# Performance work log

Measured on AMD Instinct MI355X. Metric: run time of the kernel, lower is better.

The kernel has to match this reference:

```python
import jax, jax.numpy as jnp
import numpy as np

EPS = 1e-5
NUM_HEADS = 8
MASK_FILL = -50000.0


def set_norm(X, fmask):
    # Masked "set" layer-norm: mean/var over ALL valid (row, feature) entries
    # of each set jointly. fmask: [B, S, 1] float (1 = valid row).
    D = X.shape[-1]
    cnt = fmask.sum(axis=(1, 2), keepdims=True) * D
    mean = (X * fmask).sum(axis=(1, 2), keepdims=True) / cnt
    var = (((X - mean) ** 2) * fmask).sum(axis=(1, 2), keepdims=True) / cnt
    return (X - mean) / jnp.sqrt(var + EPS) * fmask


def setup_inputs() -> dict:
    key = jax.random.key(0)
    ks = jax.random.split(key, 9)
    B, S, D = 8, 1024, 512
    Q = jax.random.normal(ks[0], (B, S, D), dtype=jnp.float32)
    Q = Q.at[:, 3 * S // 4:, :].set(0.0)
    scale = 0.02
    params = {
        'Wq': jax.random.normal(ks[1], (D, D), jnp.float32) * scale,
        'bq': jnp.zeros((D,), jnp.float32),
        'Wk': jax.random.normal(ks[2], (D, D), jnp.float32) * scale,
        'bk': jnp.zeros((D,), jnp.float32),
        'Wv': jax.random.normal(ks[3], (D, D), jnp.float32) * scale,
        'bv': jnp.zeros((D,), jnp.float32),
        'Wo': jax.random.normal(ks[4], (D, D), jnp.float32) * scale,
        'bo': jnp.zeros((D,), jnp.float32),
    }
    return {'Q': Q, **params}


def reference(Q, Wq, bq, Wk, bk, Wv, bv, Wo, bo):
    B, S, D = Q.shape
    H = NUM_HEADS
    hd = D // H

    # row mask: row is valid if any feature is nonzero
    row_valid = jnp.any(Q != 0, axis=-1, keepdims=True)      # [B, S, 1] bool
    fmask = row_valid.astype(Q.dtype)                        # [B, S, 1]

    # pre-norms (self-attention: K = V = Q)
    Qn = set_norm(Q, fmask)
    Kn = Qn

    # projections, re-masked
    Qp = (Qn @ Wq + bq) * fmask
    Kp = (Kn @ Wk + bk) * fmask
    Vp = (Kn @ Wv + bv) * fmask

    def to_heads(X):  # [B, S, D] -> [B, H, S, hd]
        return X.reshape(B, S, H, hd).transpose(0, 2, 1, 3)

    q, k, v = to_heads(Qp), to_heads(Kp), to_heads(Vp)

    # attn_mask: True = masked-out pair (invalid row in Q or K)
    invalid = ~(row_valid & row_valid.transpose(0, 2, 1))    # [B, S, S]
    invalid = invalid[:, None, :, :]                         # [B, 1, S, S]

    scale = 1.0 / np.sqrt(hd).astype(np.float32)
    scores = jnp.einsum('bhqd,bhkd->bhqk', q, k) * scale
    scores = scores + jnp.where(invalid, MASK_FILL, 0.0)
    # additive fill + post-softmax multiplicative mask (nonstandard pattern)
    w = jax.nn.softmax(scores, axis=-1) * (~invalid).astype(scores.dtype)

    attn = jnp.einsum('bhqk,bhkd->bhqd', w, v)               # [B, H, S, hd]
    attn = attn.transpose(0, 2, 1, 3).reshape(B, S, D)

    attn_out = attn + Q                                      # residual with raw input
    normed = set_norm(attn_out, fmask)                       # normVO (V mask == Q mask)
    out = attn_out + jax.nn.relu(normed @ Wo + bo)           # dropout p=0 -> identity
    return out, w
```

## Files before the change

kernel.cpp:

```cpp
#include <hip/hip_runtime.h>
#include <math.h>

#define BB 8
#define SS 1024
#define DD 512
#define HH 8
#define NROWS (BB*SS)
#define EPSV 1e-5f
#define SCALE_V 0.125f

#define I_SUM1 0
#define I_SS1  8
#define I_CNT  16
#define I_MEAN1 24
#define I_INV1 32
#define I_SUM2 40
#define I_SS2  48
#define I_MEAN2 56
#define I_INV2 64
#define I_TMASK 96
#define I_KBITS 224

typedef __bf16 bf16x8 __attribute__((ext_vector_type(8)));
typedef __bf16 bf16x4 __attribute__((ext_vector_type(4)));
typedef float f32x4 __attribute__((ext_vector_type(4)));

#define MFMA16(a,b,c) __builtin_amdgcn_mfma_f32_16x16x32_bf16(a,b,c,0,0,0)

#define LDSTRIDE 40
#define ASTR 72

__global__ __launch_bounds__(128) void stats1_k(const float* __restrict__ Q,
                                                float* __restrict__ fmask,
                                                float* __restrict__ stats) {
    int row = blockIdx.x;
    int b = row >> 10;
    int t = threadIdx.x;
    float4 v = *(const float4*)(Q + ((size_t)row << 9) + (t << 2));
    float s  = v.x + v.y + v.z + v.w;
    float ss = v.x*v.x + v.y*v.y + v.z*v.z + v.w*v.w;
    int nz = (v.x != 0.f) || (v.y != 0.f) || (v.z != 0.f) || (v.w != 0.f);
    __shared__ float rs[128], rss[128];
    __shared__ int rnz[128];
    rs[t] = s; rss[t] = ss; rnz[t] = nz;
    __syncthreads();
    for (int off = 64; off > 0; off >>= 1) {
        if (t < off) { rs[t] += rs[t+off]; rss[t] += rss[t+off]; rnz[t] |= rnz[t+off]; }
        __syncthreads();
    }
    if (t == 0) {
        float f = rnz[0] ? 1.f : 0.f;
        fmask[row] = f;
        if (f != 0.f) {
            atomicAdd(&stats[I_SUM1 + b], rs[0]);
            atomicAdd(&stats[I_SS1 + b], rss[0]);
            atomicAdd(&stats[I_CNT + b], 1.f);
        }
    }
}

__global__ __launch_bounds__(128) void finalize_k(float* __restrict__ stats,
                                                  const float* __restrict__ fmask,
                                                  int osum, int oss, int ocnt,
                                                  int omean, int oinv, int dotile) {
    int t = threadIdx.x;
    if (t < BB) {
        float cntD = stats[ocnt + t] * 512.f;
        float mean = stats[osum + t] / cntD;
        float var  = stats[oss + t] / cntD - mean * mean;
        stats[omean + t] = mean;
        stats[oinv + t]  = rsqrtf(var + EPSV);
    }
    if (dotile) {
        int* ip = (int*)stats;
        const float* fr = fmask + (t << 6);
        int any = 0;
        for (int i = 0; i < 64; i += 4) {
            float4 v = *(const float4*)(fr + i);
            any |= (v.x != 0.f) | (v.y != 0.f) | (v.z != 0.f) | (v.w != 0.f);
        }
        ip[I_TMASK + t] = any;
        __syncthreads();
        if (t < BB) {
            int bits = 0;
            #pragma unroll
            for (int i = 0; i < 16; ++i)
                bits |= (ip[I_TMASK + (t << 4) + i] ? 1 : 0) << i;
            ip[I_KBITS + t] = bits;
        }
    }
}

__global__ __launch_bounds__(256) void tw_k(const float* __restrict__ Wq,
                                            const float* __restrict__ Wk,
                                            const float* __restrict__ Wv,
                                            const float* __restrict__ Wo,
                                            __bf16* __restrict__ Wt) {
    int z = blockIdx.z;
    const float* W = (z == 0) ? Wq : (z == 1) ? Wk : (z == 2) ? Wv : Wo;
    __bf16* dst = Wt + ((size_t)z << 18);
    __shared__ float tile[64][65];
    int t = threadIdx.x;
    int k0 = blockIdx.y << 6, n0 = blockIdx.x << 6;
    int r = t >> 4, c = (t & 15) << 2;
    #pragma unroll
    for (int i = 0; i < 4; ++i) {
        float4 v = *(const float4*)(W + (size_t)(k0 + r + i*16) * 512 + n0 + c);
        tile[r + i*16][c+0] = v.x; tile[r + i*16][c+1] = v.y;
        tile[r + i*16][c+2] = v.z; tile[r + i*16][c+3] = v.w;
    }
    __syncthreads();
    #pragma unroll
    for (int i = 0; i < 4; ++i) {
        int n = r + i*16;
        bf16x4 o;
        o[0] = (__bf16)tile[c+0][n]; o[1] = (__bf16)tile[c+1][n];
        o[2] = (__bf16)tile[c+2][n]; o[3] = (__bf16)tile[c+3][n];
        *(bf16x4*)(dst + (size_t)(n0 + n) * 512 + k0 + c) = o;
    }
}

__global__ __launch_bounds__(256) void projqkv_k(
    const float* __restrict__ Q, const float* __restrict__ stats,
    const float* __restrict__ fmask, const __bf16* __restrict__ Wt,
    const float* __restrict__ bq, const float* __restrict__ bk,
    const float* __restrict__ bv,
    __bf16* __restrict__ Qp, __bf16* __restrict__ Kp, __bf16* __restrict__ Vt)
{
    __shared__ __align__(16) __bf16 smem[64 * LDSTRIDE * 4];
    int t = threadIdx.x;
    int m0 = blockIdx.y << 6, n0 = blockIdx.x << 6;
    int b = m0 >> 10, s0 = m0 & 1023, h = n0 >> 6;
    int bh = (b << 3) + h;
    const int* ip = (const int*)stats;
    if (!ip[I_TMASK + (m0 >> 6)]) {
        int m = t >> 2, ch = (t & 3) << 4;
        bf16x8 z = {};
        *(bf16x8*)(Qp + ((size_t)(m0 + m) << 9) + n0 + ch)     = z;
        *(bf16x8*)(Qp + ((size_t)(m0 + m) << 9) + n0 + ch + 8) = z;
        *(bf16x8*)(Kp + ((size_t)(m0 + m) << 9) + n0 + ch)     = z;
        *(bf16x8*)(Kp + ((size_t)(m0 + m) << 9) + n0 + ch + 8) = z;
        *(bf16x8*)(Vt + ((size_t)bh << 16) + ((size_t)m << 10) + s0 + ch)     = z;
        *(bf16x8*)(Vt + ((size_t)bh << 16) + ((size_t)m << 10) + s0 + ch + 8) = z;
        return;
    }
    __bf16* As = smem;
    int srow = t >> 2, skp = (t & 3) << 3;
    int arow = m0 + srow;
    float fi   = fmask[arow] * stats[I_INV1 + b];
    float mean = stats[I_MEAN1 + b];
    int wave = t >> 6, lane = t & 63, quad = lane >> 4, l16 = lane & 15;
    int aoff  = (wave * 16 + l16) * LDSTRIDE + quad * 8;
    int boff0 = l16 * LDSTRIDE + quad * 8;
    f32x4 acc[3][4] = {};
    const float*  Arow = Q + ((size_t)arow << 9);
    const __bf16* Brow = Wt + ((size_t)(n0 + srow) << 9);
    float4 a0 = *(const float4*)(Arow + skp);
    float4 a1 = *(const float4*)(Arow + skp + 4);
    bf16x8 w0 = *(const bf16x8*)(Brow + skp);
    bf16x8 w1 = *(const bf16x8*)(Brow + (1 << 18) + skp);
    bf16x8 w2 = *(const bf16x8*)(Brow + (2 << 18) + skp);
    for (int k0 = 0; k0 < 512; k0 += 32) {
        bf16x8 av;
        av[0] = (__bf16)((a0.x - mean) * fi); av[1] = (__bf16)((a0.y - mean) * fi);
        av[2] = (__bf16)((a0.z - mean) * fi); av[3] = (__bf16)((a0.w - mean) * fi);
        av[4] = (__bf16)((a1.x - mean) * fi); av[5] = (__bf16)((a1.y - mean) * fi);
        av[6] = (__bf16)((a1.z - mean) * fi); av[7] = (__bf16)((a1.w - mean) * fi);
        *(bf16x8*)&As[srow * LDSTRIDE + skp] = av;
        *(bf16x8*)&smem[64*LDSTRIDE*1 + srow * LDSTRIDE + skp] = w0;
        *(bf16x8*)&smem[64*LDSTRIDE*2 + srow * LDSTRIDE + skp] = w1;
        *(bf16x8*)&smem[64*LDSTRIDE*3 + srow * LDSTRIDE + skp] = w2;
        __syncthreads();
        if (k0 < 480) {
            a0 = *(const float4*)(Arow + k0 + 32 + skp);
            a1 = *(const float4*)(Arow + k0 + 36 + skp);
            w0 = *(const bf16x8*)(Brow + k0 + 32 + skp);
            w1 = *(const bf16x8*)(Brow + (1 << 18) + k0 + 32 + skp);
            w2 = *(const bf16x8*)(Brow + (2 << 18) + k0 + 32 + skp);
        }
        bf16x8 af = *(const bf16x8*)&As[aoff];
        #pragma unroll
        for (int nt = 0; nt < 4; ++nt) {
            int bo = boff0 + nt * (16 * LDSTRIDE);
            acc[0][nt] = MFMA16(af, *(const bf16x8*)&smem[64*LDSTRIDE*1 + bo], acc[0][nt]);
            acc[1][nt] = MFMA16(af, *(const bf16x8*)&smem[64*LDSTRIDE*2 + bo], acc[1][nt]);
            acc[2][nt] = MFMA16(af, *(const bf16x8*)&smem[64*LDSTRIDE*3 + bo], acc[2][nt]);
        }
        __syncthreads();
    }
    float fmr[4];
    #pragma unroll
    for (int reg = 0; reg < 4; ++reg) fmr[reg] = fmask[m0 + wave*16 + quad*4 + reg];
    __bf16* Cs = smem;
    #pragma unroll
    for (int z = 0; z < 2; ++z) {
        const float* bias = z ? bk : bq;
        __bf16* C = z ? Kp : Qp;
        #pragma unroll
        for (int nt = 0; nt < 4; ++nt) {
            float bn = bias[n0 + nt * 16 + l16];
            #pragma unroll
            for (int reg = 0; reg < 4; ++reg) {
                int m = wave * 16 + quad * 4 + reg;
                Cs[m * 70 + nt * 16 + l16] = (__bf16)((acc[z][nt][reg] + bn) * fmr[reg]);
            }
        }
        __syncthreads();
        int m = t >> 2, ch = (t & 3) << 4;
        bf16x8 o0 = *(const bf16x8*)&Cs[m * 70 + ch];
        bf16x8 o1 = *(const bf16x8*)&Cs[m * 70 + ch + 8];
        *(bf16x8*)(C + ((size_t)(m0 + m) << 9) + n0 + ch)     = o0;
        *(bf16x8*)(C + ((size_t)(m0 + m) << 9) + n0 + ch + 8) = o1;
        __syncthreads();
    }
    #pragma unroll
    for (int nt = 0; nt < 4; ++nt) {
        int d = nt * 16 + l16;
        float bn = bv[n0 + d];
        #pragma unroll
        for (int reg = 0; reg < 4; ++reg) {
            int sl = wave * 16 + quad * 4 + reg;
            Cs[d * 70 + sl] = (__bf16)((acc[2][nt][reg] + bn) * fmr[reg]);
        }
    }
    __syncthreads();
    {
        int d = t >> 2, seg = (t & 3) << 4;
        bf16x8 o0 = *(const bf16x8*)&Cs[d * 70 + seg];
        bf16x8 o1 = *(const bf16x8*)&Cs[d * 70 + seg + 8];
        *(bf16x8*)(Vt + ((size_t)bh << 16) + ((size_t)d << 10) + s0 + seg)     = o0;
        *(bf16x8*)(Vt + ((size_t)bh << 16) + ((size_t)d << 10) + s0 + seg + 8) = o1;
    }
}

__global__ __launch_bounds__(256) void rowsum_k(
    const __bf16* __restrict__ Qp, const __bf16* __restrict__ Kp,
    const float* __restrict__ fmask, const float* __restrict__ stats,
    float* __restrict__ invrow)
{
    int bh = blockIdx.y, b = bh >> 3, h = bh & 7;
    int q0 = blockIdx.x << 6;
    int t = threadIdx.x;
    const int* ip = (const int*)stats;
    int kb = ip[I_KBITS + b];
    if (!((kb >> (q0 >> 6)) & 1)) {
        if (t < 64) invrow[(bh << 10) + q0 + t] = 0.f;
        return;
    }
    __shared__ __align__(16) __bf16 Qs[64 * ASTR];
    __shared__ __align__(16) __bf16 Ks[64 * ASTR];
    int wave = t >> 6, lane = t & 63, quad = lane >> 4, l16 = lane & 15;
    int fb = b << 10;
    int sr = t >> 3, sc = (t & 7) << 3;
    #pragma unroll
    for (int it = 0; it < 2; ++it) {
        int row = it * 32 + sr;
        *(bf16x8*)&Qs[row * ASTR + sc] =
            *(const bf16x8*)(Qp + ((size_t)(fb + q0 + row) << 9) + (h << 6) + sc);
    }
    __syncthreads();
    int aoff = (wave * 16 + l16) * ASTR + quad * 8;
    bf16x8 qa0 = *(const bf16x8*)&Qs[aoff];
    bf16x8 qa1 = *(const bf16x8*)&Qs[aoff + 32];
    float rsum[4] = {0.f, 0.f, 0.f, 0.f};
    bf16x8 kr0, kr1;
    bool curok = kb & 1;
    if (curok) {
        kr0 = *(const bf16x8*)(Kp + ((size_t)(fb + sr) << 9) + (h << 6) + sc);
        kr1 = *(const bf16x8*)(Kp + ((size_t)(fb + 32 + sr) << 9) + (h << 6) + sc);
    }
    for (int kc = 0; kc < 16; ++kc) {
        bool nextok = (kc < 15) && ((kb >> (kc + 1)) & 1);
        int nbase = fb + ((kc + 1) << 6);
        if (curok) {
            *(bf16x8*)&Ks[sr * ASTR + sc] = kr0;
            *(bf16x8*)&Ks[(32 + sr) * ASTR + sc] = kr1;
            __syncthreads();
            if (nextok) {
                kr0 = *(const bf16x8*)(Kp + ((size_t)(nbase + sr) << 9) + (h << 6) + sc);
                kr1 = *(const bf16x8*)(Kp + ((size_t)(nbase + 32 + sr) << 9) + (h << 6) + sc);
            }
            int kc0 = kc << 6;
            #pragma unroll
            for (int nt = 0; nt < 4; ++nt) {
                int boff = (nt * 16 + l16) * ASTR + quad * 8;
                f32x4 s = {};
                s = MFMA16(qa0, *(const bf16x8*)&Ks[boff], s);
                s = MFMA16(qa1, *(const bf16x8*)&Ks[boff + 32], s);
                float fk = fmask[fb + kc0 + nt * 16 + l16];
                #pragma unroll
                for (int r = 0; r < 4; ++r)
                    rsum[r] += (fk != 0.f) ? __expf(s[r] * SCALE_V) : 0.f;
            }
            __syncthreads();
        } else if (nextok) {
            kr0 = *(const bf16x8*)(Kp + ((size_t)(nbase + sr) << 9) + (h << 6) + sc);
            kr1 = *(const bf16x8*)(Kp + ((size_t)(nbase + 32 + sr) << 9) + (h << 6) + sc);
        }
        curok = nextok;
    }
    #pragma unroll
    for (int r = 0; r < 4; ++r) {
        float v = rsum[r];
        v += __shfl_xor(v, 1); v += __shfl_xor(v, 2);
        v += __shfl_xor(v, 4); v += __shfl_xor(v, 8);
        if (l16 == 0) {
            int q = q0 + wave * 16 + quad * 4 + r;
            float fq = fmask[fb + q];
            invrow[(bh << 10) + q] = (fq != 0.f && v > 0.f) ? 1.f / v : 0.f;
        }
    }
}

__global__ __launch_bounds__(256) void attn_k(
    const __bf16* __restrict__ Qp, const __bf16* __restrict__ Kp,
    const __bf16* __restrict__ Vt, const float* __restrict__ invrow,
    const float* __restrict__ fmask, const float* __restrict__ Q,
    float* __restrict__ stats, float* __restrict__ w, float* __restrict__ attn)
{
    int bh = blockIdx.y, b = bh >> 3, h = bh & 7;
    int q0 = blockIdx.x << 6;
    int t = threadIdx.x;
    const int* ip = (const int*)stats;
    int kb = ip[I_KBITS + b];
    int fb = b << 10;
    size_t wqbase = ((size_t)bh << 20) + ((size_t)q0 << 10);
    if (!((kb >> (q0 >> 6)) & 1)) {
        int q = t >> 2, ch = (t & 3) << 4;
        float4 z4 = {0.f, 0.f, 0.f, 0.f};
        float* wp0 = w + wqbase + ((size_t)q << 10) + ch;
        #pragma unroll
        for (int kc0 = 0; kc0 < 1024; kc0 += 64) {
            *(float4*)(wp0 + kc0)      = z4;
            *(float4*)(wp0 + kc0 + 4)  = z4;
            *(float4*)(wp0 + kc0 + 8)  = z4;
            *(float4*)(wp0 + kc0 + 12) = z4;
        }
        size_t base = ((size_t)(fb + q0 + q) << 9) + (h << 6) + ch;
        #pragma unroll
        for (int i = 0; i < 4; ++i)
            *(float4*)(attn + base + i*4) = *(const float4*)(Q + base + i*4);
        return;
    }
    __shared__ __align__(16) __bf16 Qs[64 * ASTR];
    __shared__ __align__(16) __bf16 Ks[64 * ASTR];
    __shared__ __align__(16) __bf16 Vs[64 * ASTR];
    __shared__ __align__(16) __bf16 Ws[64 * ASTR];
    int wave = t >> 6, lane = t & 63, quad = lane >> 4, l16 = lane & 15;
    int sr = t >> 3, sc = (t & 7) << 3;
    #pragma unroll
    for (int it = 0; it < 2; ++it) {
        int row = it * 32 + sr;
        *(bf16x8*)&Qs[row * ASTR + sc] =
            *(const bf16x8*)(Qp + ((size_t)(fb + q0 + row) << 9) + (h << 6) + sc);
    }
    __syncthreads();
    int aoff = (wave * 16 + l16) * ASTR + quad * 8;
    bf16x8 qa0 = *(const bf16x8*)&Qs[aoff];
    bf16x8 qa1 = *(const bf16x8*)&Qs[aoff + 32];
    float inv[4];
    #pragma unroll
    for (int r = 0; r < 4; ++r)
        inv[r] = invrow[(bh << 10) + q0 + wave * 16 + quad * 4 + r];
    f32x4 accO[4] = {};
    bf16x8 kr0, kr1, vr0, vr1;
    bool curok = kb & 1;
    if (curok) {
        kr0 = *(const bf16x8*)(Kp + ((size_t)(fb + sr) << 9) + (h << 6) + sc);
        kr1 = *(const bf16x8*)(Kp + ((size_t)(fb + 32 + sr) << 9) + (h << 6) + sc);
        vr0 = *(const bf16x8*)(Vt + ((size_t)bh << 16) + ((size_t)sr << 10) + sc);
        vr1 = *(const bf16x8*)(Vt + ((size_t)bh << 16) + ((size_t)(32 + sr) << 10) + sc);
    }
    for (int kc = 0; kc < 16; ++kc) {
        int kc0 = kc << 6;
        bool nextok = (kc < 15) && ((kb >> (kc + 1)) & 1);
        int nk0 = kc0 + 64;
        if (curok) {
            *(bf16x8*)&Ks[sr * ASTR + sc] = kr0;
            *(bf16x8*)&Ks[(32 + sr) * ASTR + sc] = kr1;
            *(bf16x8*)&Vs[sr * ASTR + sc] = vr0;
            *(bf16x8*)&Vs[(32 + sr) * ASTR + sc] = vr1;
            __syncthreads();
            if (nextok) {
                kr0 = *(const bf16x8*)(Kp + ((size_t)(fb + nk0 + sr) << 9) + (h << 6) + sc);
                kr1 = *(const bf16x8*)(Kp + ((size_t)(fb + nk0 + 32 + sr) << 9) + (h << 6) + sc);
                vr0 = *(const bf16x8*)(Vt + ((size_t)bh << 16) + ((size_t)sr << 10) + nk0 + sc);
                vr1 = *(const bf16x8*)(Vt + ((size_t)bh << 16) + ((size_t)(32 + sr) << 10) + nk0 + sc);
            }
            #pragma unroll
            for (int nt = 0; nt < 4; ++nt) {
                int boff = (nt * 16 + l16) * ASTR + quad * 8;
                f32x4 s = {};
                s = MFMA16(qa0, *(const bf16x8*)&Ks[boff], s);
                s = MFMA16(qa1, *(const bf16x8*)&Ks[boff + 32], s);
                float fk = fmask[fb + kc0 + nt * 16 + l16];
                #pragma unroll
                for (int r = 0; r < 4; ++r) {
                    float p = (fk != 0.f) ? __expf(s[r] * SCALE_V) * inv[r] : 0.f;
                    Ws[(wave * 16 + quad * 4 + r) * ASTR + nt * 16 + l16] = (__bf16)p;
                }
            }
            __syncthreads();
            bf16x8 pa0 = *(const bf16x8*)&Ws[aoff];
            bf16x8 pa1 = *(const bf16x8*)&Ws[aoff + 32];
            #pragma unroll
            for (int nt = 0; nt < 4; ++nt) {
                int boff = (nt * 16 + l16) * ASTR + quad * 8;
                accO[nt] = MFMA16(pa0, *(const bf16x8*)&Vs[boff], accO[nt]);
                accO[nt] = MFMA16(pa1, *(const bf16x8*)&Vs[boff + 32], accO[nt]);
            }
            {
                int q = t >> 2, ch = (t & 3) << 4;
                bf16x8 w0 = *(const bf16x8*)&Ws[q * ASTR + ch];
                bf16x8 w1 = *(const bf16x8*)&Ws[q * ASTR + ch + 8];
                float4 f0, f1, f2, f3;
                f0.x = (float)w0[0]; f0.y = (float)w0[1]; f0.z = (float)w0[2]; f0.w = (float)w0[3];
                f1.x = (float)w0[4]; f1.y = (float)w0[5]; f1.z = (float)w0[6]; f1.w = (float)w0[7];
                f2.x = (float)w1[0]; f2.y = (float)w1[1]; f2.z = (float)w1[2]; f2.w = (float)w1[3];
                f3.x = (float)w1[4]; f3.y = (float)w1[5]; f3.z = (float)w1[6]; f3.w = (float)w1[7];
                float* wp = w + wqbase + ((size_t)q << 10) + kc0 + ch;
                *(float4*)(wp)      = f0;
                *(float4*)(wp + 4)  = f1;
                *(float4*)(wp + 8)  = f2;
                *(float4*)(wp + 12) = f3;
            }
            __syncthreads();
        } else {
            int q = t >> 2, ch = (t & 3) << 4;
            float4 z4 = {0.f, 0.f, 0.f, 0.f};
            float* wp = w + wqbase + ((size_t)q << 10) + kc0 + ch;
            *(float4*)(wp)      = z4;
            *(float4*)(wp + 4)  = z4;
            *(float4*)(wp + 8)  = z4;
            *(float4*)(wp + 12) = z4;
            if (nextok) {
                kr0 = *(const bf16x8*)(Kp + ((size_t)(fb + nk0 + sr) << 9) + (h << 6) + sc);
                kr1 = *(const bf16x8*)(Kp + ((size_t)(fb + nk0 + 32 + sr) << 9) + (h << 6) + sc);
                vr0 = *(const bf16x8*)(Vt + ((size_t)bh << 16) + ((size_t)sr << 10) + nk0 + sc);
                vr1 = *(const bf16x8*)(Vt + ((size_t)bh << 16) + ((size_t)(32 + sr) << 10) + nk0 + sc);
            }
        }
        curok = nextok;
    }
    float s1 = 0.f, s2 = 0.f;
    #pragma unroll
    for (int nt = 0; nt < 4; ++nt) {
        int d = nt * 16 + l16;
        #pragma unroll
        for (int r = 0; r < 4; ++r) {
            int q = q0 + wave * 16 + quad * 4 + r;
            size_t off = ((size_t)(fb + q) << 9) + (h << 6) + d;
            float v = accO[nt][r] + Q[off];
            attn[off] = v;
            s1 += v; s2 += v * v;
        }
    }
    #pragma unroll
    for (int o = 32; o > 0; o >>= 1) {
        s1 += __shfl_xor(s1, o);
        s2 += __shfl_xor(s2, o);
    }
    float* red = (float*)Qs;
    if (lane == 0) { red[wave * 2] = s1; red[wave * 2 + 1] = s2; }
    __syncthreads();
    if (t == 0) {
        atomicAdd(&stats[I_SUM2 + b], red[0] + red[2] + red[4] + red[6]);
        atomicAdd(&stats[I_SS2 + b], red[1] + red[3] + red[5] + red[7]);
    }
}

__global__ __launch_bounds__(256) void final_gemm(
    const float* __restrict__ attn, const float* __restrict__ stats,
    const float* __restrict__ fmask, const __bf16* __restrict__ Wot,
    const float* __restrict__ bo, float* __restrict__ out)
{
    int t = threadIdx.x;
    int m0 = blockIdx.y << 6, n0 = blockIdx.x << 6;
    const int* ip = (const int*)stats;
    if (!ip[I_TMASK + (m0 >> 6)]) {
        int m = t >> 2, c = (t & 3) << 4;
        size_t base = ((size_t)(m0 + m) << 9) + n0 + c;
        #pragma unroll
        for (int i = 0; i < 4; ++i) {
            float4 a = *(const float4*)(attn + base + i * 4);
            float4 bb = *(const float4*)(bo + n0 + c + i * 4);
            float4 o;
            o.x = a.x + fmaxf(bb.x, 0.f); o.y = a.y + fmaxf(bb.y, 0.f);
            o.z = a.z + fmaxf(bb.z, 0.f); o.w = a.w + fmaxf(bb.w, 0.f);
            *(float4*)(out + base + i * 4) = o;
        }
        return;
    }
    __shared__ __align__(16) __bf16 smem[64 * LDSTRIDE * 2];
    __bf16* As = smem;
    __bf16* Bs = smem + 64 * LDSTRIDE;
    int srow = t >> 2, skp = (t & 3) << 3;
    int arow = m0 + srow, ab = arow >> 10;
    float fi   = fmask[arow] * stats[I_INV2 + ab];
    float mean = stats[I_MEAN2 + ab];
    int wave = t >> 6, lane = t & 63, quad = lane >> 4, l16 = lane & 15;
    int aoff  = (wave * 16 + l16) * LDSTRIDE + quad * 8;
    int boff0 = l16 * LDSTRIDE + quad * 8;
    f32x4 acc[4] = {};
    const float*  Arow = attn + ((size_t)arow << 9);
    const __bf16* Brow = Wot + ((size_t)(n0 + srow) << 9);
    float4 a0 = *(const float4*)(Arow + skp);
    float4 a1 = *(const float4*)(Arow + skp + 4);
    bf16x8 bw = *(const bf16x8*)(Brow + skp);
    for (int k0 = 0; k0 < 512; k0 += 32) {
        bf16x8 av;
        av[0] = (__bf16)((a0.x - mean) * fi); av[1] = (__bf16)((a0.y - mean) * fi);
        av[2] = (__bf16)((a0.z - mean) * fi); av[3] = (__bf16)((a0.w - mean) * fi);
        av[4] = (__bf16)((a1.x - mean) * fi); av[5] = (__bf16)((a1.y - mean) * fi);
        av[6] = (__bf16)((a1.z - mean) * fi); av[7] = (__bf16)((a1.w - mean) * fi);
        *(bf16x8*)&As[srow * LDSTRIDE + skp] = av;
        *(bf16x8*)&Bs[srow * LDSTRIDE + skp] = bw;
        __syncthreads();
        if (k0 < 480) {
            a0 = *(const float4*)(Arow + k0 + 32 + skp);
            a1 = *(const float4*)(Arow + k0 + 36 + skp);
            bw = *(const bf16x8*)(Brow + k0 + 32 + skp);
        }
        bf16x8 af = *(const bf16x8*)&As[aoff];
        #pragma unroll
        for (int nt = 0; nt < 4; ++nt)
            acc[nt] = MFMA16(af, *(const bf16x8*)&Bs[boff0 + nt * (16 * LDSTRIDE)], acc[nt]);
        __syncthreads();
    }
    #pragma unroll
    for (int nt = 0; nt < 4; ++nt) {
        int n = n0 + nt * 16 + l16;
        float bn = bo[n];
        #pragma unroll
        for (int reg = 0; reg < 4; ++reg) {
            int m = m0 + wave * 16 + quad * 4 + reg;
            size_t off = ((size_t)m << 9) + n;
            out[off] = attn[off] + fmaxf(acc[nt][reg] + bn, 0.f);
        }
    }
}

extern "C" void kernel_launch(void* const* d_in, const int* in_sizes, int n_in,
                              void* d_out, int out_size, void* d_ws, size_t ws_size,
                              hipStream_t stream) {
    const float* Q  = (const float*)d_in[0];
    const float* Wq = (const float*)d_in[1];
    const float* bq = (const float*)d_in[2];
    const float* Wk = (const float*)d_in[3];
    const float* bk = (const float*)d_in[4];
    const float* Wv = (const float*)d_in[5];
    const float* bv = (const float*)d_in[6];
    const float* Wo = (const float*)d_in[7];
    const float* bo = (const float*)d_in[8];
    float* out = (float*)d_out;
    float* w   = out + (size_t)BB * SS * DD;

    char* ws = (char*)d_ws;
    float* stats  = (float*)ws;
    float* fmask  = (float*)(ws + 4096);
    float* invrow = (float*)(ws + 4096 + 32768);
    __bf16* Wt = (__bf16*)(ws + 299008);
    __bf16* Qp = Wt + ((size_t)4 << 18);
    __bf16* Kp = Qp + ((size_t)NROWS * DD);
    __bf16* Vt = Kp + ((size_t)NROWS * DD);
    float* attn = (float*)(Vt + ((size_t)NROWS * DD));

    (void)hipMemsetAsync(stats, 0, 4096, stream);
    stats1_k<<<NROWS, 128, 0, stream>>>(Q, fmask, stats);
    finalize_k<<<1, 128, 0, stream>>>(stats, fmask, I_SUM1, I_SS1, I_CNT, I_MEAN1, I_INV1, 1);
    tw_k<<<dim3(8, 8, 4), 256, 0, stream>>>(Wq, Wk, Wv, Wo, Wt);
    projqkv_k<<<dim3(8, 128), 256, 0, stream>>>(Q, stats, fmask, Wt,
                                                bq, bk, bv, Qp, Kp, Vt);
    rowsum_k<<<dim3(16, 64), 256, 0, stream>>>(Qp, Kp, fmask, stats, invrow);
    attn_k<<<dim3(16, 64), 256, 0, stream>>>(Qp, Kp, Vt, invrow, fmask, Q, stats, w, attn);
    finalize_k<<<1, 128, 0, stream>>>(stats, fmask, I_SUM2, I_SS2, I_CNT, I_MEAN2, I_INV2, 0);
    final_gemm<<<dim3(8, 128), 256, 0, stream>>>(attn, stats, fmask,
                                                 Wt + ((size_t)3 << 18), bo, out);
}
```

Measured before the change: 600.9 us.

## Load MFMA operands directly from global memory and use nontemporal output stores

```diff
diff --git a/kernel.cpp b/kernel.cpp
--- a/kernel.cpp
+++ b/kernel.cpp
@@ -27,7 +27,6 @@
 
 #define MFMA16(a,b,c) __builtin_amdgcn_mfma_f32_16x16x32_bf16(a,b,c,0,0,0)
 
-#define LDSTRIDE 40
 #define ASTR 72
 
 __global__ __launch_bounds__(128) void stats1_k(const float* __restrict__ Q,
@@ -127,7 +126,7 @@
     const float* __restrict__ bv,
     __bf16* __restrict__ Qp, __bf16* __restrict__ Kp, __bf16* __restrict__ Vt)
 {
-    __shared__ __align__(16) __bf16 smem[64 * LDSTRIDE * 4];
+    __shared__ __align__(16) __bf16 Cs[64 * 70];
     int t = threadIdx.x;
     int m0 = blockIdx.y << 6, n0 = blockIdx.x << 6;
     int b = m0 >> 10, s0 = m0 & 1023, h = n0 >> 6;
@@ -144,54 +143,32 @@
         *(bf16x8*)(Vt + ((size_t)bh << 16) + ((size_t)m << 10) + s0 + ch + 8) = z;
         return;
     }
-    __bf16* As = smem;
-    int srow = t >> 2, skp = (t & 3) << 3;
-    int arow = m0 + srow;
+    int wave = t >> 6, lane = t & 63, quad = lane >> 4, l16 = lane & 15;
+    int arow = m0 + wave * 16 + l16;
     float fi   = fmask[arow] * stats[I_INV1 + b];
     float mean = stats[I_MEAN1 + b];
-    int wave = t >> 6, lane = t & 63, quad = lane >> 4, l16 = lane & 15;
-    int aoff  = (wave * 16 + l16) * LDSTRIDE + quad * 8;
-    int boff0 = l16 * LDSTRIDE + quad * 8;
+    const float*  Ar = Q + ((size_t)arow << 9) + (quad << 3);
+    const __bf16* Br = Wt + ((size_t)(n0 + l16) << 9) + (quad << 3);
     f32x4 acc[3][4] = {};
-    const float*  Arow = Q + ((size_t)arow << 9);
-    const __bf16* Brow = Wt + ((size_t)(n0 + srow) << 9);
-    float4 a0 = *(const float4*)(Arow + skp);
-    float4 a1 = *(const float4*)(Arow + skp + 4);
-    bf16x8 w0 = *(const bf16x8*)(Brow + skp);
-    bf16x8 w1 = *(const bf16x8*)(Brow + (1 << 18) + skp);
-    bf16x8 w2 = *(const bf16x8*)(Brow + (2 << 18) + skp);
     for (int k0 = 0; k0 < 512; k0 += 32) {
-        bf16x8 av;
-        av[0] = (__bf16)((a0.x - mean) * fi); av[1] = (__bf16)((a0.y - mean) * fi);
-        av[2] = (__bf16)((a0.z - mean) * fi); av[3] = (__bf16)((a0.w - mean) * fi);
-        av[4] = (__bf16)((a1.x - mean) * fi); av[5] = (__bf16)((a1.y - mean) * fi);
-        av[6] = (__bf16)((a1.z - mean) * fi); av[7] = (__bf16)((a1.w - mean) * fi);
-        *(bf16x8*)&As[srow * LDSTRIDE + skp] = av;
-        *(bf16x8*)&smem[64*LDSTRIDE*1 + srow * LDSTRIDE + skp] = w0;
-        *(bf16x8*)&smem[64*LDSTRIDE*2 + srow * LDSTRIDE + skp] = w1;
-        *(bf16x8*)&smem[64*LDSTRIDE*3 + srow * LDSTRIDE + skp] = w2;
-        __syncthreads();
-        if (k0 < 480) {
-            a0 = *(const float4*)(Arow + k0 + 32 + skp);
-            a1 = *(const float4*)(Arow + k0 + 36 + skp);
-            w0 = *(const bf16x8*)(Brow + k0 + 32 + skp);
-            w1 = *(const bf16x8*)(Brow + (1 << 18) + k0 + 32 + skp);
-            w2 = *(const bf16x8*)(Brow + (2 << 18) + k0 + 32 + skp);
-        }
-        bf16x8 af = *(const bf16x8*)&As[aoff];
+        float4 a0 = *(const float4*)(Ar + k0);
+        float4 a1 = *(const float4*)(Ar + k0 + 4);
+        bf16x8 af;
+        af[0] = (__bf16)((a0.x - mean) * fi); af[1] = (__bf16)((a0.y - mean) * fi);
+        af[2] = (__bf16)((a0.z - mean) * fi); af[3] = (__bf16)((a0.w - mean) * fi);
+        af[4] = (__bf16)((a1.x - mean) * fi); af[5] = (__bf16)((a1.y - mean) * fi);
+        af[6] = (__bf16)((a1.z - mean) * fi); af[7] = (__bf16)((a1.w - mean) * fi);
         #pragma unroll
         for (int nt = 0; nt < 4; ++nt) {
-            int bo = boff0 + nt * (16 * LDSTRIDE);
-            acc[0][nt] = MFMA16(af, *(const bf16x8*)&smem[64*LDSTRIDE*1 + bo], acc[0][nt]);
-            acc[1][nt] = MFMA16(af, *(const bf16x8*)&smem[64*LDSTRIDE*2 + bo], acc[1][nt]);
-            acc[2][nt] = MFMA16(af, *(const bf16x8*)&smem[64*LDSTRIDE*3 + bo], acc[2][nt]);
-        }
-        __syncthreads();
+            const __bf16* bp = Br + nt * (16 * 512) + k0;
+            acc[0][nt] = MFMA16(af, *(const bf16x8*)(bp),           acc[0][nt]);
+            acc[1][nt] = MFMA16(af, *(const bf16x8*)(bp + (1<<18)), acc[1][nt]);
+            acc[2][nt] = MFMA16(af, *(const bf16x8*)(bp + (2<<18)), acc[2][nt]);
+        }
     }
     float fmr[4];
     #pragma unroll
     for (int reg = 0; reg < 4; ++reg) fmr[reg] = fmask[m0 + wave*16 + quad*4 + reg];
-    __bf16* Cs = smem;
     #pragma unroll
     for (int z = 0; z < 2; ++z) {
         const float* bias = z ? bk : bq;
@@ -247,57 +224,26 @@
         if (t < 64) invrow[(bh << 10) + q0 + t] = 0.f;
         return;
     }
-    __shared__ __align__(16) __bf16 Qs[64 * ASTR];
-    __shared__ __align__(16) __bf16 Ks[64 * ASTR];
     int wave = t >> 6, lane = t & 63, quad = lane >> 4, l16 = lane & 15;
     int fb = b << 10;
-    int sr = t >> 3, sc = (t & 7) << 3;
-    #pragma unroll
-    for (int it = 0; it < 2; ++it) {
-        int row = it * 32 + sr;
-        *(bf16x8*)&Qs[row * ASTR + sc] =
-            *(const bf16x8*)(Qp + ((size_t)(fb + q0 + row) << 9) + (h << 6) + sc);
-    }
-    __syncthreads();
-    int aoff = (wave * 16 + l16) * ASTR + quad * 8;
-    bf16x8 qa0 = *(const bf16x8*)&Qs[aoff];
-    bf16x8 qa1 = *(const bf16x8*)&Qs[aoff + 32];
+    const __bf16* Qr = Qp + ((size_t)(fb + q0 + wave*16 + l16) << 9) + (h << 6) + (quad << 3);
+    bf16x8 qa0 = *(const bf16x8*)(Qr);
+    bf16x8 qa1 = *(const bf16x8*)(Qr + 32);
     float rsum[4] = {0.f, 0.f, 0.f, 0.f};
-    bf16x8 kr0, kr1;
-    bool curok = kb & 1;
-    if (curok) {
-        kr0 = *(const bf16x8*)(Kp + ((size_t)(fb + sr) << 9) + (h << 6) + sc);
-        kr1 = *(const bf16x8*)(Kp + ((size_t)(fb + 32 + sr) << 9) + (h << 6) + sc);
-    }
     for (int kc = 0; kc < 16; ++kc) {
-        bool nextok = (kc < 15) && ((kb >> (kc + 1)) & 1);
-        int nbase = fb + ((kc + 1) << 6);
-        if (curok) {
-            *(bf16x8*)&Ks[sr * ASTR + sc] = kr0;
-            *(bf16x8*)&Ks[(32 + sr) * ASTR + sc] = kr1;
-            __syncthreads();
-            if (nextok) {
-                kr0 = *(const bf16x8*)(Kp + ((size_t)(nbase + sr) << 9) + (h << 6) + sc);
-                kr1 = *(const bf16x8*)(Kp + ((size_t)(nbase + 32 + sr) << 9) + (h << 6) + sc);
-            }
-            int kc0 = kc << 6;
+        if (!((kb >> kc) & 1)) continue;
+        int kc0 = kc << 6;
+        #pragma unroll
+        for (int nt = 0; nt < 4; ++nt) {
+            const __bf16* Kr = Kp + ((size_t)(fb + kc0 + nt*16 + l16) << 9) + (h << 6) + (quad << 3);
+            f32x4 s = {};
+            s = MFMA16(qa0, *(const bf16x8*)(Kr), s);
+            s = MFMA16(qa1, *(const bf16x8*)(Kr + 32), s);
+            float fk = fmask[fb + kc0 + nt * 16 + l16];
             #pragma unroll
-            for (int nt = 0; nt < 4; ++nt) {
-                int boff = (nt * 16 + l16) * ASTR + quad * 8;
-                f32x4 s = {};
-                s = MFMA16(qa0, *(const bf16x8*)&Ks[boff], s);
-                s = MFMA16(qa1, *(const bf16x8*)&Ks[boff + 32], s);
-                float fk = fmask[fb + kc0 + nt * 16 + l16];
-                #pragma unroll
-                for (int r = 0; r < 4; ++r)
-                    rsum[r] += (fk != 0.f) ? __expf(s[r] * SCALE_V) : 0.f;
-            }
-            __syncthreads();
-        } else if (nextok) {
-            kr0 = *(const bf16x8*)(Kp + ((size_t)(nbase + sr) << 9) + (h << 6) + sc);
-            kr1 = *(const bf16x8*)(Kp + ((size_t)(nbase + 32 + sr) << 9) + (h << 6) + sc);
-        }
-        curok = nextok;
+            for (int r = 0; r < 4; ++r)
+                rsum[r] += (fk != 0.f) ? __expf(s[r] * SCALE_V) : 0.f;
+        }
     }
     #pragma unroll
     for (int r = 0; r < 4; ++r) {
@@ -327,14 +273,14 @@
     size_t wqbase = ((size_t)bh << 20) + ((size_t)q0 << 10);
     if (!((kb >> (q0 >> 6)) & 1)) {
         int q = t >> 2, ch = (t & 3) << 4;
-        float4 z4 = {0.f, 0.f, 0.f, 0.f};
+        f32x4 z4 = {0.f, 0.f, 0.f, 0.f};
         float* wp0 = w + wqbase + ((size_t)q << 10) + ch;
         #pragma unroll
         for (int kc0 = 0; kc0 < 1024; kc0 += 64) {
-            *(float4*)(wp0 + kc0)      = z4;
-            *(float4*)(wp0 + kc0 + 4)  = z4;
-            *(float4*)(wp0 + kc0 + 8)  = z4;
-            *(float4*)(wp0 + kc0 + 12) = z4;
+            __builtin_nontemporal_store(z4, (f32x4*)(wp0 + kc0));
+            __builtin_nontemporal_store(z4, (f32x4*)(wp0 + kc0 + 4));
+            __builtin_nontemporal_store(z4, (f32x4*)(wp0 + kc0 + 8));
+            __builtin_nontemporal_store(z4, (f32x4*)(wp0 + kc0 + 12));
         }
         size_t base = ((size_t)(fb + q0 + q) << 9) + (h << 6) + ch;
         #pragma unroll
@@ -342,57 +288,27 @@
             *(float4*)(attn + base + i*4) = *(const float4*)(Q + base + i*4);
         return;
     }
-    __shared__ __align__(16) __bf16 Qs[64 * ASTR];
-    __shared__ __align__(16) __bf16 Ks[64 * ASTR];
-    __shared__ __align__(16) __bf16 Vs[64 * ASTR];
     __shared__ __align__(16) __bf16 Ws[64 * ASTR];
+    __shared__ float red[8];
     int wave = t >> 6, lane = t & 63, quad = lane >> 4, l16 = lane & 15;
-    int sr = t >> 3, sc = (t & 7) << 3;
-    #pragma unroll
-    for (int it = 0; it < 2; ++it) {
-        int row = it * 32 + sr;
-        *(bf16x8*)&Qs[row * ASTR + sc] =
-            *(const bf16x8*)(Qp + ((size_t)(fb + q0 + row) << 9) + (h << 6) + sc);
-    }
-    __syncthreads();
-    int aoff = (wave * 16 + l16) * ASTR + quad * 8;
-    bf16x8 qa0 = *(const bf16x8*)&Qs[aoff];
-    bf16x8 qa1 = *(const bf16x8*)&Qs[aoff + 32];
+    const __bf16* Qr = Qp + ((size_t)(fb + q0 + wave*16 + l16) << 9) + (h << 6) + (quad << 3);
+    bf16x8 qa0 = *(const bf16x8*)(Qr);
+    bf16x8 qa1 = *(const bf16x8*)(Qr + 32);
     float inv[4];
     #pragma unroll
     for (int r = 0; r < 4; ++r)
         inv[r] = invrow[(bh << 10) + q0 + wave * 16 + quad * 4 + r];
     f32x4 accO[4] = {};
-    bf16x8 kr0, kr1, vr0, vr1;
-    bool curok = kb & 1;
-    if (curok) {
-        kr0 = *(const bf16x8*)(Kp + ((size_t)(fb + sr) << 9) + (h << 6) + sc);
-        kr1 = *(const bf16x8*)(Kp + ((size_t)(fb + 32 + sr) << 9) + (h << 6) + sc);
-        vr0 = *(const bf16x8*)(Vt + ((size_t)bh << 16) + ((size_t)sr << 10) + sc);
-        vr1 = *(const bf16x8*)(Vt + ((size_t)bh << 16) + ((size_t)(32 + sr) << 10) + sc);
-    }
+    int aoff = (wave * 16 + l16) * ASTR + (quad << 3);
     for (int kc = 0; kc < 16; ++kc) {
         int kc0 = kc << 6;
-        bool nextok = (kc < 15) && ((kb >> (kc + 1)) & 1);
-        int nk0 = kc0 + 64;
-        if (curok) {
-            *(bf16x8*)&Ks[sr * ASTR + sc] = kr0;
-            *(bf16x8*)&Ks[(32 + sr) * ASTR + sc] = kr1;
-            *(bf16x8*)&Vs[sr * ASTR + sc] = vr0;
-            *(bf16x8*)&Vs[(32 + sr) * ASTR + sc] = vr1;
-            __syncthreads();
-            if (nextok) {
-                kr0 = *(const bf16x8*)(Kp + ((size_t)(fb + nk0 + sr) << 9) + (h << 6) + sc);
-                kr1 = *(const bf16x8*)(Kp + ((size_t)(fb + nk0 + 32 + sr) << 9) + (h << 6) + sc);
-                vr0 = *(const bf16x8*)(Vt + ((size_t)bh << 16) + ((size_t)sr << 10) + nk0 + sc);
-                vr1 = *(const bf16x8*)(Vt + ((size_t)bh << 16) + ((size_t)(32 + sr) << 10) + nk0 + sc);
-            }
+        if ((kb >> kc) & 1) {
             #pragma unroll
             for (int nt = 0; nt < 4; ++nt) {
-                int boff = (nt * 16 + l16) * ASTR + quad * 8;
+                const __bf16* Kr = Kp + ((size_t)(fb + kc0 + nt*16 + l16) << 9) + (h << 6) + (quad << 3);
                 f32x4 s = {};
-                s = MFMA16(qa0, *(const bf16x8*)&Ks[boff], s);
-                s = MFMA16(qa1, *(const bf16x8*)&Ks[boff + 32], s);
+                s = MFMA16(qa0, *(const bf16x8*)(Kr), s);
+                s = MFMA16(qa1, *(const bf16x8*)(Kr + 32), s);
                 float fk = fmask[fb + kc0 + nt * 16 + l16];
                 #pragma unroll
                 for (int r = 0; r < 4; ++r) {
@@ -405,42 +321,35 @@
             bf16x8 pa1 = *(const bf16x8*)&Ws[aoff + 32];
             #pragma unroll
             for (int nt = 0; nt < 4; ++nt) {
-                int boff = (nt * 16 + l16) * ASTR + quad * 8;
-                accO[nt] = MFMA16(pa0, *(const bf16x8*)&Vs[boff], accO[nt]);
-                accO[nt] = MFMA16(pa1, *(const bf16x8*)&Vs[boff + 32], accO[nt]);
+                const __bf16* Vr = Vt + ((size_t)bh << 16) + ((size_t)(nt*16 + l16) << 10) + kc0 + (quad << 3);
+                accO[nt] = MFMA16(pa0, *(const bf16x8*)(Vr), accO[nt]);
+                accO[nt] = MFMA16(pa1, *(const bf16x8*)(Vr + 32), accO[nt]);
             }
             {
                 int q = t >> 2, ch = (t & 3) << 4;
                 bf16x8 w0 = *(const bf16x8*)&Ws[q * ASTR + ch];
                 bf16x8 w1 = *(const bf16x8*)&Ws[q * ASTR + ch + 8];
-                float4 f0, f1, f2, f3;
-                f0.x = (float)w0[0]; f0.y = (float)w0[1]; f0.z = (float)w0[2]; f0.w = (float)w0[3];
-                f1.x = (float)w0[4]; f1.y = (float)w0[5]; f1.z = (float)w0[6]; f1.w = (float)w0[7];
-                f2.x = (float)w1[0]; f2.y = (float)w1[1]; f2.z = (float)w1[2]; f2.w = (float)w1[3];
-                f3.x = (float)w1[4]; f3.y = (float)w1[5]; f3.z = (float)w1[6]; f3.w = (float)w1[7];
+                f32x4 f0, f1, f2, f3;
+                f0[0] = (float)w0[0]; f0[1] = (float)w0[1]; f0[2] = (float)w0[2]; f0[3] = (float)w0[3];
+                f1[0] = (float)w0[4]; f1[1] = (float)w0[5]; f1[2] = (float)w0[6]; f1[3] = (float)w0[7];
+                f2[0] = (float)w1[0]; f2[1] = (float)w1[1]; f2[2] = (float)w1[2]; f2[3] = (float)w1[3];
+                f3[0] = (float)w1[4]; f3[1] = (float)w1[5]; f3[2] = (float)w1[6]; f3[3] = (float)w1[7];
                 float* wp = w + wqbase + ((size_t)q << 10) + kc0 + ch;
-                *(float4*)(wp)      = f0;
-                *(float4*)(wp + 4)  = f1;
-                *(float4*)(wp + 8)  = f2;
-                *(float4*)(wp + 12) = f3;
+                __builtin_nontemporal_store(f0, (f32x4*)(wp));
+                __builtin_nontemporal_store(f1, (f32x4*)(wp + 4));
+                __builtin_nontemporal_store(f2, (f32x4*)(wp + 8));
+                __builtin_nontemporal_store(f3, (f32x4*)(wp + 12));
             }
             __syncthreads();
         } else {
             int q = t >> 2, ch = (t & 3) << 4;
-            float4 z4 = {0.f, 0.f, 0.f, 0.f};
+            f32x4 z4 = {0.f, 0.f, 0.f, 0.f};
             float* wp = w + wqbase + ((size_t)q << 10) + kc0 + ch;
-            *(float4*)(wp)      = z4;
-            *(float4*)(wp + 4)  = z4;
-            *(float4*)(wp + 8)  = z4;
-            *(float4*)(wp + 12) = z4;
-            if (nextok) {
-                kr0 = *(const bf16x8*)(Kp + ((size_t)(fb + nk0 + sr) << 9) + (h << 6) + sc);
-                kr1 = *(const bf16x8*)(Kp + ((size_t)(fb + nk0 + 32 + sr) << 9) + (h << 6) + sc);
-                vr0 = *(const bf16x8*)(Vt + ((size_t)bh << 16) + ((size_t)sr << 10) + nk0 + sc);
-                vr1 = *(const bf16x8*)(Vt + ((size_t)bh << 16) + ((size_t)(32 + sr) << 10) + nk0 + sc);
-            }
-        }
-        curok = nextok;
+            __builtin_nontemporal_store(z4, (f32x4*)(wp));
+            __builtin_nontemporal_store(z4, (f32x4*)(wp + 4));
+            __builtin_nontemporal_store(z4, (f32x4*)(wp + 8));
+            __builtin_nontemporal_store(z4, (f32x4*)(wp + 12));
+        }
     }
     float s1 = 0.f, s2 = 0.f;
     #pragma unroll
@@ -460,7 +369,6 @@
         s1 += __shfl_xor(s1, o);
         s2 += __shfl_xor(s2, o);
     }
-    float* red = (float*)Qs;
     if (lane == 0) { red[wave * 2] = s1; red[wave * 2 + 1] = s2; }
     __syncthreads();
     if (t == 0) {
@@ -484,48 +392,31 @@
         for (int i = 0; i < 4; ++i) {
             float4 a = *(const float4*)(attn + base + i * 4);
             float4 bb = *(const float4*)(bo + n0 + c + i * 4);
-            float4 o;
-            o.x = a.x + fmaxf(bb.x, 0.f); o.y = a.y + fmaxf(bb.y, 0.f);
-            o.z = a.z + fmaxf(bb.z, 0.f); o.w = a.w + fmaxf(bb.w, 0.f);
-            *(float4*)(out + base + i * 4) = o;
+            f32x4 o;
+            o[0] = a.x + fmaxf(bb.x, 0.f); o[1] = a.y + fmaxf(bb.y, 0.f);
+            o[2] = a.z + fmaxf(bb.z, 0.f); o[3] = a.w + fmaxf(bb.w, 0.f);
+            __builtin_nontemporal_store(o, (f32x4*)(out + base + i * 4));
         }
         return;
     }
-    __shared__ __align__(16) __bf16 smem[64 * LDSTRIDE * 2];
-    __bf16* As = smem;
-    __bf16* Bs = smem + 64 * LDSTRIDE;
-    int srow = t >> 2, skp = (t & 3) << 3;
-    int arow = m0 + srow, ab = arow >> 10;
+    int wave = t >> 6, lane = t & 63, quad = lane >> 4, l16 = lane & 15;
+    int arow = m0 + wave * 16 + l16, ab = arow >> 10;
     float fi   = fmask[arow] * stats[I_INV2 + ab];
     float mean = stats[I_MEAN2 + ab];
-    int wave = t >> 6, lane = t & 63, quad = lane >> 4, l16 = lane & 15;
-    int aoff  = (wave * 16 + l16) * LDSTRIDE + quad * 8;
-    int boff0 = l16 * LDSTRIDE + quad * 8;
+    const float*  Ar = attn + ((size_t)arow << 9) + (quad << 3);
+    const __bf16* Br = Wot + ((size_t)(n0 + l16) << 9) + (quad << 3);
     f32x4 acc[4] = {};
-    const float*  Arow = attn + ((size_t)arow << 9);
-    const __bf16* Brow = Wot + ((size_t)(n0 + srow) << 9);
-    float4 a0 = *(const float4*)(Arow + skp);
-    float4 a1 = *(const float4*)(Arow + skp + 4);
-    bf16x8 bw = *(const bf16x8*)(Brow + skp);
     for (int k0 = 0; k0 < 512; k0 += 32) {
-        bf16x8 av;
-        av[0] = (__bf16)((a0.x - mean) * fi); av[1] = (__bf16)((a0.y - mean) * fi);
-        av[2] = (__bf16)((a0.z - mean) * fi); av[3] = (__bf16)((a0.w - mean) * fi);
-        av[4] = (__bf16)((a1.x - mean) * fi); av[5] = (__bf16)((a1.y - mean) * fi);
-        av[6] = (__bf16)((a1.z - mean) * fi); av[7] = (__bf16)((a1.w - mean) * fi);
-        *(bf16x8*)&As[srow * LDSTRIDE + skp] = av;
-        *(bf16x8*)&Bs[srow * LDSTRIDE + skp] = bw;
-        __syncthreads();
-        if (k0 < 480) {
-            a0 = *(const float4*)(Arow + k0 + 32 + skp);
-            a1 = *(const float4*)(Arow + k0 + 36 + skp);
-            bw = *(const bf16x8*)(Brow + k0 + 32 + skp);
-        }
-        bf16x8 af = *(const bf16x8*)&As[aoff];
+        float4 a0 = *(const float4*)(Ar + k0);
+        float4 a1 = *(const float4*)(Ar + k0 + 4);
+        bf16x8 af;
+        af[0] = (__bf16)((a0.x - mean) * fi); af[1] = (__bf16)((a0.y - mean) * fi);
+        af[2] = (__bf16)((a0.z - mean) * fi); af[3] = (__bf16)((a0.w - mean) * fi);
+        af[4] = (__bf16)((a1.x - mean) * fi); af[5] = (__bf16)((a1.y - mean) * fi);
+        af[6] = (__bf16)((a1.z - mean) * fi); af[7] = (__bf16)((a1.w - mean) * fi);
         #pragma unroll
         for (int nt = 0; nt < 4; ++nt)
-            acc[nt] = MFMA16(af, *(const bf16x8*)&Bs[boff0 + nt * (16 * LDSTRIDE)], acc[nt]);
-        __syncthreads();
+            acc[nt] = MFMA16(af, *(const bf16x8*)(Br + nt * (16 * 512) + k0), acc[nt]);
     }
     #pragma unroll
     for (int nt = 0; nt < 4; ++nt) {
@@ -535,7 +426,8 @@
         for (int reg = 0; reg < 4; ++reg) {
             int m = m0 + wave * 16 + quad * 4 + reg;
             size_t off = ((size_t)m << 9) + n;
-            out[off] = attn[off] + fmaxf(acc[nt][reg] + bn, 0.f);
+            float v = attn[off] + fmaxf(acc[nt][reg] + bn, 0.f);
+            __builtin_nontemporal_store(v, &out[off]);
         }
     }
 }
```

After: 990.3 us. +64.8%, slower.

## Fuse softmax row-sum pass into attention kernel and load Q fragments directly

Applied to the files above, without the earlier changes.

```diff
diff --git a/kernel.cpp b/kernel.cpp
--- a/kernel.cpp
+++ b/kernel.cpp
@@ -233,88 +233,9 @@
     }
 }
 
-__global__ __launch_bounds__(256) void rowsum_k(
-    const __bf16* __restrict__ Qp, const __bf16* __restrict__ Kp,
-    const float* __restrict__ fmask, const float* __restrict__ stats,
-    float* __restrict__ invrow)
-{
-    int bh = blockIdx.y, b = bh >> 3, h = bh & 7;
-    int q0 = blockIdx.x << 6;
-    int t = threadIdx.x;
-    const int* ip = (const int*)stats;
-    int kb = ip[I_KBITS + b];
-    if (!((kb >> (q0 >> 6)) & 1)) {
-        if (t < 64) invrow[(bh << 10) + q0 + t] = 0.f;
-        return;
-    }
-    __shared__ __align__(16) __bf16 Qs[64 * ASTR];
-    __shared__ __align__(16) __bf16 Ks[64 * ASTR];
-    int wave = t >> 6, lane = t & 63, quad = lane >> 4, l16 = lane & 15;
-    int fb = b << 10;
-    int sr = t >> 3, sc = (t & 7) << 3;
-    #pragma unroll
-    for (int it = 0; it < 2; ++it) {
-        int row = it * 32 + sr;
-        *(bf16x8*)&Qs[row * ASTR + sc] =
-            *(const bf16x8*)(Qp + ((size_t)(fb + q0 + row) << 9) + (h << 6) + sc);
-    }
-    __syncthreads();
-    int aoff = (wave * 16 + l16) * ASTR + quad * 8;
-    bf16x8 qa0 = *(const bf16x8*)&Qs[aoff];
-    bf16x8 qa1 = *(const bf16x8*)&Qs[aoff + 32];
-    float rsum[4] = {0.f, 0.f, 0.f, 0.f};
-    bf16x8 kr0, kr1;
-    bool curok = kb & 1;
-    if (curok) {
-        kr0 = *(const bf16x8*)(Kp + ((size_t)(fb + sr) << 9) + (h << 6) + sc);
-        kr1 = *(const bf16x8*)(Kp + ((size_t)(fb + 32 + sr) << 9) + (h << 6) + sc);
-    }
-    for (int kc = 0; kc < 16; ++kc) {
-        bool nextok = (kc < 15) && ((kb >> (kc + 1)) & 1);
-        int nbase = fb + ((kc + 1) << 6);
-        if (curok) {
-            *(bf16x8*)&Ks[sr * ASTR + sc] = kr0;
-            *(bf16x8*)&Ks[(32 + sr) * ASTR + sc] = kr1;
-            __syncthreads();
-            if (nextok) {
-                kr0 = *(const bf16x8*)(Kp + ((size_t)(nbase + sr) << 9) + (h << 6) + sc);
-                kr1 = *(const bf16x8*)(Kp + ((size_t)(nbase + 32 + sr) << 9) + (h << 6) + sc);
-            }
-            int kc0 = kc << 6;
-            #pragma unroll
-            for (int nt = 0; nt < 4; ++nt) {
-                int boff = (nt * 16 + l16) * ASTR + quad * 8;
-                f32x4 s = {};
-                s = MFMA16(qa0, *(const bf16x8*)&Ks[boff], s);
-                s = MFMA16(qa1, *(const bf16x8*)&Ks[boff + 32], s);
-                float fk = fmask[fb + kc0 + nt * 16 + l16];
-                #pragma unroll
-                for (int r = 0; r < 4; ++r)
-                    rsum[r] += (fk != 0.f) ? __expf(s[r] * SCALE_V) : 0.f;
-            }
-            __syncthreads();
-        } else if (nextok) {
-            kr0 = *(const bf16x8*)(Kp + ((size_t)(nbase + sr) << 9) + (h << 6) + sc);
-            kr1 = *(const bf16x8*)(Kp + ((size_t)(nbase + 32 + sr) << 9) + (h << 6) + sc);
-        }
-        curok = nextok;
-    }
-    #pragma unroll
-    for (int r = 0; r < 4; ++r) {
-        float v = rsum[r];
-        v += __shfl_xor(v, 1); v += __shfl_xor(v, 2);
-        v += __shfl_xor(v, 4); v += __shfl_xor(v, 8);
-        if (l16 == 0) {
-            int q = q0 + wave * 16 + quad * 4 + r;
-            float fq = fmask[fb + q];
-            invrow[(bh << 10) + q] = (fq != 0.f && v > 0.f) ? 1.f / v : 0.f;
-        }
-    }
-}
-
 __global__ __launch_bounds__(256) void attn_k(
     const __bf16* __restrict__ Qp, const __bf16* __restrict__ Kp,
-    const __bf16* __restrict__ Vt, const float* __restrict__ invrow,
+    const __bf16* __restrict__ Vt,
     const float* __restrict__ fmask, const float* __restrict__ Q,
     float* __restrict__ stats, float* __restrict__ w, float* __restrict__ attn)
 {
@@ -342,29 +263,67 @@
             *(float4*)(attn + base + i*4) = *(const float4*)(Q + base + i*4);
         return;
     }
-    __shared__ __align__(16) __bf16 Qs[64 * ASTR];
     __shared__ __align__(16) __bf16 Ks[64 * ASTR];
     __shared__ __align__(16) __bf16 Vs[64 * ASTR];
     __shared__ __align__(16) __bf16 Ws[64 * ASTR];
+    __shared__ float red[8];
     int wave = t >> 6, lane = t & 63, quad = lane >> 4, l16 = lane & 15;
     int sr = t >> 3, sc = (t & 7) << 3;
-    #pragma unroll
-    for (int it = 0; it < 2; ++it) {
-        int row = it * 32 + sr;
-        *(bf16x8*)&Qs[row * ASTR + sc] =
-            *(const bf16x8*)(Qp + ((size_t)(fb + q0 + row) << 9) + (h << 6) + sc);
-    }
-    __syncthreads();
-    int aoff = (wave * 16 + l16) * ASTR + quad * 8;
-    bf16x8 qa0 = *(const bf16x8*)&Qs[aoff];
-    bf16x8 qa1 = *(const bf16x8*)&Qs[aoff + 32];
+    const __bf16* Qr = Qp + ((size_t)(fb + q0 + wave*16 + l16) << 9) + (h << 6) + (quad << 3);
+    bf16x8 qa0 = *(const bf16x8*)(Qr);
+    bf16x8 qa1 = *(const bf16x8*)(Qr + 32);
+    int aoff = (wave * 16 + l16) * ASTR + (quad << 3);
+
+    float rsum[4] = {0.f, 0.f, 0.f, 0.f};
+    bf16x8 kr0, kr1;
+    bool curok = kb & 1;
+    if (curok) {
+        kr0 = *(const bf16x8*)(Kp + ((size_t)(fb + sr) << 9) + (h << 6) + sc);
+        kr1 = *(const bf16x8*)(Kp + ((size_t)(fb + 32 + sr) << 9) + (h << 6) + sc);
+    }
+    for (int kc = 0; kc < 16; ++kc) {
+        bool nextok = (kc < 15) && ((kb >> (kc + 1)) & 1);
+        int nbase = fb + ((kc + 1) << 6);
+        if (curok) {
+            *(bf16x8*)&Ks[sr * ASTR + sc] = kr0;
+            *(bf16x8*)&Ks[(32 + sr) * ASTR + sc] = kr1;
+            __syncthreads();
+            if (nextok) {
+                kr0 = *(const bf16x8*)(Kp + ((size_t)(nbase + sr) << 9) + (h << 6) + sc);
+                kr1 = *(const bf16x8*)(Kp + ((size_t)(nbase + 32 + sr) << 9) + (h << 6) + sc);
+            }
+            int kc0 = kc << 6;
+            #pragma unroll
+            for (int nt = 0; nt < 4; ++nt) {
+                int boff = (nt * 16 + l16) * ASTR + (quad << 3);
+                f32x4 s = {};
+                s = MFMA16(qa0, *(const bf16x8*)&Ks[boff], s);
+                s = MFMA16(qa1, *(const bf16x8*)&Ks[boff + 32], s);
+                float fk = fmask[fb + kc0 + nt * 16 + l16];
+                #pragma unroll
+                for (int r = 0; r < 4; ++r)
+                    rsum[r] += (fk != 0.f) ? __expf(s[r] * SCALE_V) : 0.f;
+            }
+            __syncthreads();
+        } else if (nextok) {
+            kr0 = *(const bf16x8*)(Kp + ((size_t)(nbase + sr) << 9) + (h << 6) + sc);
+            kr1 = *(const bf16x8*)(Kp + ((size_t)(nbase + 32 + sr) << 9) + (h << 6) + sc);
+        }
+        curok = nextok;
+    }
     float inv[4];
     #pragma unroll
-    for (int r = 0; r < 4; ++r)
-        inv[r] = invrow[(bh << 10) + q0 + wave * 16 + quad * 4 + r];
+    for (int r = 0; r < 4; ++r) {
+        float v = rsum[r];
+        v += __shfl_xor(v, 1); v += __shfl_xor(v, 2);
+        v += __shfl_xor(v, 4); v += __shfl_xor(v, 8);
+        float fq = fmask[fb + q0 + wave * 16 + quad * 4 + r];
+        inv[r] = (fq != 0.f && v > 0.f) ? 1.f / v : 0.f;
+    }
+
     f32x4 accO[4] = {};
-    bf16x8 kr0, kr1, vr0, vr1;
-    bool curok = kb & 1;
+    bf16x8 vr0, vr1;
+    curok = kb & 1;
     if (curok) {
         kr0 = *(const bf16x8*)(Kp + ((size_t)(fb + sr) << 9) + (h << 6) + sc);
         kr1 = *(const bf16x8*)(Kp + ((size_t)(fb + 32 + sr) << 9) + (h << 6) + sc);
@@ -389,7 +348,7 @@
             }
             #pragma unroll
             for (int nt = 0; nt < 4; ++nt) {
-                int boff = (nt * 16 + l16) * ASTR + quad * 8;
+                int boff = (nt * 16 + l16) * ASTR + (quad << 3);
                 f32x4 s = {};
                 s = MFMA16(qa0, *(const bf16x8*)&Ks[boff], s);
                 s = MFMA16(qa1, *(const bf16x8*)&Ks[boff + 32], s);
@@ -405,7 +364,7 @@
             bf16x8 pa1 = *(const bf16x8*)&Ws[aoff + 32];
             #pragma unroll
             for (int nt = 0; nt < 4; ++nt) {
-                int boff = (nt * 16 + l16) * ASTR + quad * 8;
+                int boff = (nt * 16 + l16) * ASTR + (quad << 3);
                 accO[nt] = MFMA16(pa0, *(const bf16x8*)&Vs[boff], accO[nt]);
                 accO[nt] = MFMA16(pa1, *(const bf16x8*)&Vs[boff + 32], accO[nt]);
             }
@@ -460,7 +419,6 @@
         s1 += __shfl_xor(s1, o);
         s2 += __shfl_xor(s2, o);
     }
-    float* red = (float*)Qs;
     if (lane == 0) { red[wave * 2] = s1; red[wave * 2 + 1] = s2; }
     __syncthreads();
     if (t == 0) {
@@ -558,8 +516,7 @@
     char* ws = (char*)d_ws;
     float* stats  = (float*)ws;
     float* fmask  = (float*)(ws + 4096);
-    float* invrow = (float*)(ws + 4096 + 32768);
-    __bf16* Wt = (__bf16*)(ws + 299008);
+    __bf16* Wt = (__bf16*)(ws + 4096 + 32768);
     __bf16* Qp = Wt + ((size_t)4 << 18);
     __bf16* Kp = Qp + ((size_t)NROWS * DD);
     __bf16* Vt = Kp + ((size_t)NROWS * DD);
@@ -571,8 +528,7 @@
     tw_k<<<dim3(8, 8, 4), 256, 0, stream>>>(Wq, Wk, Wv, Wo, Wt);
     projqkv_k<<<dim3(8, 128), 256, 0, stream>>>(Q, stats, fmask, Wt,
                                                 bq, bk, bv, Qp, Kp, Vt);
-    rowsum_k<<<dim3(16, 64), 256, 0, stream>>>(Qp, Kp, fmask, stats, invrow);
-    attn_k<<<dim3(16, 64), 256, 0, stream>>>(Qp, Kp, Vt, invrow, fmask, Q, stats, w, attn);
+    attn_k<<<dim3(16, 64), 256, 0, stream>>>(Qp, Kp, Vt, fmask, Q, stats, w, attn);
     finalize_k<<<1, 128, 0, stream>>>(stats, fmask, I_SUM2, I_SS2, I_CNT, I_MEAN2, I_INV2, 0);
     final_gemm<<<dim3(8, 128), 256, 0, stream>>>(attn, stats, fmask,
                                                  Wt + ((size_t)3 << 18), bo, out);
```

Measured after the change: 589.0 us. -2.0%, faster.
